# Kernel tuning notes

Hardware: AMD Instinct MI355X
Metric: run time of the kernel (lower is better)

Reference implementation:

```python
import jax, jax.numpy as jnp
import numpy as np

N = 50000

def gcn_conv(x, W, b, src, dst, n):
    # x: [N, Fin], W: [Fin, Fout]; PyG GCNConv: transform then sym-normalized aggregate (self-loops included in src/dst)
    h = x @ W  # [N, Fout]
    deg = jax.ops.segment_sum(jnp.ones_like(dst, dtype=h.dtype), dst, num_segments=n)
    inv_sqrt = jnp.where(deg > 0, jax.lax.rsqrt(deg), 0.0)
    norm = inv_sqrt[src] * inv_sqrt[dst]  # [E+N]
    msg = h[src] * norm[:, None]
    out = jax.ops.segment_sum(msg, dst, num_segments=n)
    return out + b


def setup_inputs() -> dict:
    key = jax.random.key(0)
    ks = jax.random.split(key, 8)
    d_in, d_h, n_exp, E = 64, 64, 16, 800000
    x = jax.random.normal(ks[0], (N, d_in), dtype=jnp.float32)
    edge_index = jax.random.randint(ks[1], (2, E), 0, N, dtype=jnp.int64)
    s = 1.0 / np.sqrt(d_in)
    W1 = jax.random.uniform(ks[2], (d_in, d_h), minval=-s, maxval=s, dtype=jnp.float32)
    b1 = jnp.zeros((d_h,), jnp.float32)
    W2 = jax.random.uniform(ks[3], (d_h, d_h), minval=-s, maxval=s, dtype=jnp.float32)
    b2 = jnp.zeros((d_h,), jnp.float32)
    Wc = jax.random.uniform(ks[4], (d_h, n_exp), minval=-s, maxval=s, dtype=jnp.float32)
    bc = jnp.zeros((n_exp,), jnp.float32)
    return {"x": x, "edge_index": edge_index, "W1": W1, "b1": b1, "W2": W2, "b2": b2, "Wc": Wc, "bc": bc}


def reference(x, edge_index, W1, b1, W2, b2, Wc, bc):
    # add self-loops once (PyG GCNConv default add_self_loops=True)
    loops = jnp.arange(N, dtype=edge_index.dtype)
    src = jnp.concatenate([edge_index[0], loops])
    dst = jnp.concatenate([edge_index[1], loops])
    h = jax.nn.relu(gcn_conv(x, W1, b1, src, dst, N))
    # dropout is identity in eval mode
    h = jax.nn.relu(gcn_conv(h, W2, b2, src, dst, N))
    return h @ Wc + bc
```

## Files before the change

### kernel.cpp

```cpp
#include <hip/hip_runtime.h>
#include <hip/hip_fp16.h>


#define FDIM 64
#define NCLS 16
#define TILE 2048

__global__ __launch_bounds__(256) void k_histB(const int* __restrict__ dst, int E,
                                               int* __restrict__ H) {
    __shared__ int h[256];
    int t = threadIdx.x, blk = blockIdx.x;
    h[t] = 0;
    __syncthreads();
    int i0 = blk * TILE;
#pragma unroll
    for (int k = 0; k < TILE / 256; ++k) {
        int i = i0 + k * 256 + t;
        if (i < E) atomicAdd(&h[dst[i] >> 8], 1);
    }
    __syncthreads();
    H[blk * 256 + t] = h[t];
}

__global__ __launch_bounds__(512) void k_scanH(int* __restrict__ H, int nblk, int* __restrict__ btot) {
    __shared__ int s[512];
    int t = threadIdx.x, b = blockIdx.x;
    int v = (t < nblk) ? H[t * 256 + b] : 0;
    s[t] = v;
    __syncthreads();
    for (int off = 1; off < 512; off <<= 1) {
        int add = (t >= off) ? s[t - off] : 0;
        __syncthreads();
        s[t] += add;
        __syncthreads();
    }
    if (t < nblk) H[t * 256 + b] = s[t] - v;
    if (t == 511) btot[b] = s[511];
}

__global__ __launch_bounds__(256) void k_scatA(const int* __restrict__ src, const int* __restrict__ dst,
                                               int E, const int* __restrict__ H,
                                               const int* __restrict__ btot, int nb,
                                               unsigned* __restrict__ tmp) {
    __shared__ int s[256];
    __shared__ int Hb[256];
    __shared__ int c2[256];
    int t = threadIdx.x, blk = blockIdx.x;
    int v = (t < nb) ? btot[t] : 0;
    s[t] = v;
    __syncthreads();
    for (int off = 1; off < 256; off <<= 1) {
        int add = (t >= off) ? s[t - off] : 0;
        __syncthreads();
        s[t] += add;
        __syncthreads();
    }
    Hb[t] = (s[t] - v) + H[blk * 256 + t];
    c2[t] = 0;
    __syncthreads();
    int i0 = blk * TILE;
#pragma unroll
    for (int k = 0; k < TILE / 256; ++k) {
        int i = i0 + k * 256 + t;
        if (i < E) {
            int sv = src[i], d = dst[i];
            int b = d >> 8;
            unsigned rec = ((unsigned)(d & 255) << 16) | (unsigned)sv;
            int pos = Hb[b] + atomicAdd(&c2[b], 1);
            tmp[pos] = rec;
        }
    }
}

#define COLCAP 8192
__global__ __launch_bounds__(256) void k_binB(const unsigned* __restrict__ tmp,
                                              const int* __restrict__ btot, int nb,
                                              int n, int E, int* __restrict__ row_ptr,
                                              float* __restrict__ inv,
                                              unsigned short* __restrict__ col) {
    __shared__ int dcnt[256], s[256], cur[256];
    __shared__ unsigned short colbuf[COLCAP];
    int t = threadIdx.x, b = blockIdx.x;
    int v = (t < nb) ? btot[t] : 0;
    s[t] = v;
    __syncthreads();
    for (int off = 1; off < 256; off <<= 1) {
        int add = (t >= off) ? s[t - off] : 0;
        __syncthreads();
        s[t] += add;
        __syncthreads();
    }
    __shared__ int baseS;
    if (t == b) baseS = s[t] - v;
    dcnt[t] = 0;
    __syncthreads();
    int base = baseS;
    int cntE = btot[b];
    int node0 = b << 8;
    int nn = min(256, n - node0);
    for (int i = t; i < cntE; i += 256) atomicAdd(&dcnt[tmp[base + i] >> 16], 1);
    __syncthreads();
    int deg = dcnt[t];
    s[t] = deg;
    __syncthreads();
    for (int off = 1; off < 256; off <<= 1) {
        int add = (t >= off) ? s[t - off] : 0;
        __syncthreads();
        s[t] += add;
        __syncthreads();
    }
    int excl = s[t] - deg;
    if (t < nn) {
        row_ptr[node0 + t] = base + excl;
        inv[node0 + t] = rsqrtf((float)(deg + 1));
    }
    if (b == 0 && t == 0) row_ptr[n] = E;
    cur[t] = excl;
    __syncthreads();
    for (int i = t; i < cntE; i += 256) {
        unsigned r = tmp[base + i];
        int pos = atomicAdd(&cur[r >> 16], 1);
        unsigned short vv = (unsigned short)(r & 0xFFFFu);
        if (pos < COLCAP) colbuf[pos] = vv;
        else col[base + pos] = vv;
    }
    __syncthreads();
    int lim = min(cntE, COLCAP);
    for (int i = t; i < lim; i += 256) col[base + i] = colbuf[i];
}

__global__ __launch_bounds__(256) void k_gemm64(const float* __restrict__ X, const float* __restrict__ W,
                                                const float* __restrict__ inv, __half* __restrict__ Yh, int n) {
    __shared__ float Ws[FDIM * FDIM];
    int t = threadIdx.x;
    for (int i = t; i < FDIM * FDIM; i += 256) Ws[i] = W[i];
    __syncthreads();
    int idx = blockIdx.x * 256 + t;
    int row = idx >> 2;
    int cg = (idx & 3) * 16;
    if (row >= n) return;
    const float4* xr = (const float4*)(X + row * FDIM);
    float4 xv[16];
#pragma unroll
    for (int i = 0; i < 16; ++i) xv[i] = xr[i];
    float acc[16];
#pragma unroll
    for (int c = 0; c < 16; ++c) acc[c] = 0.f;
#pragma unroll
    for (int i = 0; i < 16; ++i) {
        float xs[4] = {xv[i].x, xv[i].y, xv[i].z, xv[i].w};
#pragma unroll
        for (int j = 0; j < 4; ++j) {
            float xk = xs[j];
            const float* wr = &Ws[(i * 4 + j) * FDIM + cg];
#pragma unroll
            for (int c = 0; c < 16; ++c) acc[c] += xk * wr[c];
        }
    }
    float iv = inv[row];
    unsigned u[8];
#pragma unroll
    for (int i = 0; i < 8; ++i) {
        __half2 hp = __floats2half2_rn(acc[2 * i] * iv, acc[2 * i + 1] * iv);
        u[i] = *(unsigned*)&hp;
    }
    uint4* yo = (uint4*)(Yh + (size_t)row * FDIM + cg);
    yo[0] = make_uint4(u[0], u[1], u[2], u[3]);
    yo[1] = make_uint4(u[4], u[5], u[6], u[7]);
}

__global__ __launch_bounds__(256) void k_aggF1(const __half* __restrict__ Ph, const float* __restrict__ inv,
                                               const int* __restrict__ row_ptr,
                                               const unsigned short* __restrict__ col,
                                               const float* __restrict__ bias,
                                               const float* __restrict__ W2,
                                               __half* __restrict__ P2, int n) {
    __shared__ float W2s[FDIM * FDIM];
    __shared__ float rbuf[16][FDIM + 1];
    int t = threadIdx.x;
    for (int i = t; i < FDIM * FDIM; i += 256) W2s[i] = W2[i];
    int lane = t & 63;
    int sub = lane >> 4;
    int fl = lane & 15;
    int wid = t >> 6;
    int nl = wid * 4 + sub;
    int node = blockIdx.x * 16 + nl;
    bool alive = node < n;
    int nodeC = alive ? node : (n - 1);
    float iv = inv[nodeC];
    const uint2* Pq = (const uint2*)Ph;
    uint2 selfq = Pq[(size_t)nodeC * 16 + fl];
    float2 sf0 = __half22float2(*(__half2*)&selfq.x);
    float2 sf1 = __half22float2(*(__half2*)&selfq.y);
    float4 acc = make_float4(sf0.x, sf0.y, sf1.x, sf1.y);
    int s = row_ptr[nodeC];
    int e = alive ? row_ptr[nodeC + 1] : s;
    int dmax = e - s;
    dmax = max(dmax, __shfl_xor(dmax, 16, 64));
    dmax = max(dmax, __shfl_xor(dmax, 32, 64));
    for (int j = 0; j < dmax; j += 8) {
        int c[8];
        float wk[8];
        uint2 q[8];
#pragma unroll
        for (int k = 0; k < 8; ++k) {
            int jj = s + j + k;
            bool ok = jj < e;
            c[k] = col[ok ? jj : s];
            wk[k] = ok ? 1.f : 0.f;
        }
#pragma unroll
        for (int k = 0; k < 8; ++k) q[k] = Pq[(size_t)c[k] * 16 + fl];
#pragma unroll
        for (int k = 0; k < 8; ++k) {
            float2 f0 = __half22float2(*(__half2*)&q[k].x);
            float2 f1 = __half22float2(*(__half2*)&q[k].y);
            acc.x = fmaf(wk[k], f0.x, acc.x);
            acc.y = fmaf(wk[k], f0.y, acc.y);
            acc.z = fmaf(wk[k], f1.x, acc.z);
            acc.w = fmaf(wk[k], f1.y, acc.w);
        }
    }
    float4 bb = ((const float4*)bias)[fl];
    rbuf[nl][fl * 4 + 0] = fmaxf(fmaf(iv, acc.x, bb.x), 0.f);
    rbuf[nl][fl * 4 + 1] = fmaxf(fmaf(iv, acc.y, bb.y), 0.f);
    rbuf[nl][fl * 4 + 2] = fmaxf(fmaf(iv, acc.z, bb.z), 0.f);
    rbuf[nl][fl * 4 + 3] = fmaxf(fmaf(iv, acc.w, bb.w), 0.f);
    __syncthreads();
    int nl2 = t >> 4;
    int cg = t & 15;
    int node2 = blockIdx.x * 16 + nl2;
    const float* rr = rbuf[nl2];
    float a0 = 0.f, a1 = 0.f, a2 = 0.f, a3 = 0.f;
#pragma unroll
    for (int i = 0; i < FDIM; ++i) {
        float xk = rr[i];
        const float* wv = &W2s[i * FDIM + cg * 4];
        a0 = fmaf(xk, wv[0], a0);
        a1 = fmaf(xk, wv[1], a1);
        a2 = fmaf(xk, wv[2], a2);
        a3 = fmaf(xk, wv[3], a3);
    }
    if (node2 < n) {
        float iv2 = inv[node2];
        __half2 h0 = __floats2half2_rn(a0 * iv2, a1 * iv2);
        __half2 h1 = __floats2half2_rn(a2 * iv2, a3 * iv2);
        uint2 val = make_uint2(*(unsigned*)&h0, *(unsigned*)&h1);
        ((uint2*)P2)[(size_t)node2 * 16 + cg] = val;
    }
}

__global__ __launch_bounds__(256) void k_aggF2(const __half* __restrict__ Ph, const float* __restrict__ inv,
                                               const int* __restrict__ row_ptr,
                                               const unsigned short* __restrict__ col,
                                               const float* __restrict__ bias,
                                               const float* __restrict__ Wc, const float* __restrict__ bc,
                                               float* __restrict__ out, int n) {
    __shared__ float WcT[NCLS * FDIM];
    int t = threadIdx.x;
    for (int i = t; i < FDIM * NCLS; i += 256) {
        int c = i & 15, f = i >> 4;
        WcT[c * FDIM + f] = Wc[i];
    }
    __syncthreads();
    int lane = t & 63;
    int sub = lane >> 4;
    int fl = lane & 15;
    int wid = t >> 6;
    int node = blockIdx.x * 16 + wid * 4 + sub;
    bool alive = node < n;
    int nodeC = alive ? node : (n - 1);
    float iv = inv[nodeC];
    const uint2* Pq = (const uint2*)Ph;
    uint2 selfq = Pq[(size_t)nodeC * 16 + fl];
    float2 sf0 = __half22float2(*(__half2*)&selfq.x);
    float2 sf1 = __half22float2(*(__half2*)&selfq.y);
    float4 acc = make_float4(sf0.x, sf0.y, sf1.x, sf1.y);
    int s = row_ptr[nodeC];
    int e = alive ? row_ptr[nodeC + 1] : s;
    int dmax = e - s;
    dmax = max(dmax, __shfl_xor(dmax, 16, 64));
    dmax = max(dmax, __shfl_xor(dmax, 32, 64));
    for (int j = 0; j < dmax; j += 8) {
        int c[8];
        float wk[8];
        uint2 q[8];
#pragma unroll
        for (int k = 0; k < 8; ++k) {
            int jj = s + j + k;
            bool ok = jj < e;
            c[k] = col[ok ? jj : s];
            wk[k] = ok ? 1.f : 0.f;
        }
#pragma unroll
        for (int k = 0; k < 8; ++k) q[k] = Pq[(size_t)c[k] * 16 + fl];
#pragma unroll
        for (int k = 0; k < 8; ++k) {
            float2 f0 = __half22float2(*(__half2*)&q[k].x);
            float2 f1 = __half22float2(*(__half2*)&q[k].y);
            acc.x = fmaf(wk[k], f0.x, acc.x);
            acc.y = fmaf(wk[k], f0.y, acc.y);
            acc.z = fmaf(wk[k], f1.x, acc.z);
            acc.w = fmaf(wk[k], f1.y, acc.w);
        }
    }
    float4 bb = ((const float4*)bias)[fl];
    float4 r;
    r.x = fmaxf(fmaf(iv, acc.x, bb.x), 0.f);
    r.y = fmaxf(fmaf(iv, acc.y, bb.y), 0.f);
    r.z = fmaxf(fmaf(iv, acc.z, bb.z), 0.f);
    r.w = fmaxf(fmaf(iv, acc.w, bb.w), 0.f);
    float part[NCLS];
#pragma unroll
    for (int c = 0; c < NCLS; ++c) {
        float4 wv = ((const float4*)(WcT + c * FDIM))[fl];
        part[c] = fmaf(r.x, wv.x, fmaf(r.y, wv.y, fmaf(r.z, wv.z, r.w * wv.w)));
    }
#pragma unroll
    for (int m = 1; m < 16; m <<= 1) {
#pragma unroll
        for (int c = 0; c < NCLS; ++c) part[c] += __shfl_xor(part[c], m, 64);
    }
    if (alive && fl < 4) {
        float4 bb2 = ((const float4*)bc)[fl];
        float4 o = make_float4(part[fl * 4 + 0] + bb2.x, part[fl * 4 + 1] + bb2.y,
                               part[fl * 4 + 2] + bb2.z, part[fl * 4 + 3] + bb2.w);
        ((float4*)out)[(size_t)node * 4 + fl] = o;
    }
}

static inline size_t align256(size_t x) { return (x + 255) & ~(size_t)255; }

extern "C" void kernel_launch(void* const* d_in, const int* in_sizes, int n_in,
                              void* d_out, int out_size, void* d_ws, size_t ws_size,
                              hipStream_t stream) {
    const float* x  = (const float*)d_in[0];
    const int*   ei = (const int*)d_in[1];
    const float* W1 = (const float*)d_in[2];
    const float* b1 = (const float*)d_in[3];
    const float* W2 = (const float*)d_in[4];
    const float* b2 = (const float*)d_in[5];
    const float* Wc = (const float*)d_in[6];
    const float* bc = (const float*)d_in[7];
    float* out = (float*)d_out;

    const int n = in_sizes[0] / FDIM;
    const int E = in_sizes[1] / 2;
    const int* src = ei;
    const int* dst = ei + E;

    const int nb = (n + 255) >> 8;
    const int nblk = (E + TILE - 1) / TILE;

    char* w = (char*)d_ws;
    size_t off = 0;
    int* H = (int*)(w + off);        off = align256(off + (size_t)nblk * 256 * 4);
    int* btot = (int*)(w + off);     off = align256(off + 256 * 4);
    int* row_ptr = (int*)(w + off);  off = align256(off + (size_t)(n + 1) * 4);
    float* inv = (float*)(w + off);  off = align256(off + (size_t)n * 4);
    unsigned* tmp = (unsigned*)(w + off);             off = align256(off + (size_t)E * 4);
    unsigned short* col = (unsigned short*)(w + off); off = align256(off + (size_t)(E + 8) * 2);
    __half* P1 = (__half*)(w + off); off = align256(off + (size_t)n * FDIM * 2);
    __half* P2 = (__half*)(w + off); off = align256(off + (size_t)n * FDIM * 2);
    (void)ws_size;

    const int nbG = (n * 4 + 255) / 256;
    const int nbA = (n + 15) / 16;

    k_histB<<<nblk, 256, 0, stream>>>(dst, E, H);
    k_scanH<<<nb, 512, 0, stream>>>(H, nblk, btot);
    k_scatA<<<nblk, 256, 0, stream>>>(src, dst, E, H, btot, nb, tmp);
    k_binB<<<nb, 256, 0, stream>>>(tmp, btot, nb, n, E, row_ptr, inv, col);

    k_gemm64<<<nbG, 256, 0, stream>>>(x, W1, inv, P1, n);
    k_aggF1<<<nbA, 256, 0, stream>>>(P1, inv, row_ptr, col, b1, W2, P2, n);
    k_aggF2<<<nbA, 256, 0, stream>>>(P2, inv, row_ptr, col, b2, Wc, bc, out, n);
}
```

Before: 162.8 us.

## Merge first-layer GEMM into histogram kernel, apply source normalization in aggregation

The first GEMM no longer scales rows by inv-sqrt degree, so it no longer depends on the CSR build. It is folded into the histogram launch as extra blocks, letting GEMM work overlap the edge histogram and removing one launch. In exchange, the first aggregation now gathers inv[c] for every neighbor edge, adding a random 4-byte load per edge. Both aggregation loops also drop the wavefront-wide max-degree shuffle and loop per 16-lane group on its own degree, so lanes within a wave may diverge.

```diff
diff --git a/kernel.cpp b/kernel.cpp
--- a/kernel.cpp
+++ b/kernel.cpp
@@ -6,20 +6,60 @@
 #define NCLS 16
 #define TILE 2048
 
-__global__ __launch_bounds__(256) void k_histB(const int* __restrict__ dst, int E,
-                                               int* __restrict__ H) {
+__global__ __launch_bounds__(256) void k_histgemm(const int* __restrict__ dst, int E,
+                                                  int* __restrict__ H, int nblk,
+                                                  const float* __restrict__ X,
+                                                  const float* __restrict__ W,
+                                                  __half* __restrict__ Yh, int n) {
+    __shared__ float Ws[FDIM * FDIM];
     __shared__ int h[256];
     int t = threadIdx.x, blk = blockIdx.x;
-    h[t] = 0;
-    __syncthreads();
-    int i0 = blk * TILE;
-#pragma unroll
-    for (int k = 0; k < TILE / 256; ++k) {
-        int i = i0 + k * 256 + t;
-        if (i < E) atomicAdd(&h[dst[i] >> 8], 1);
-    }
-    __syncthreads();
-    H[blk * 256 + t] = h[t];
+    if (blk < nblk) {
+        h[t] = 0;
+        __syncthreads();
+        int i0 = blk * TILE;
+#pragma unroll
+        for (int k = 0; k < TILE / 256; ++k) {
+            int i = i0 + k * 256 + t;
+            if (i < E) atomicAdd(&h[dst[i] >> 8], 1);
+        }
+        __syncthreads();
+        H[blk * 256 + t] = h[t];
+    } else {
+        for (int i = t; i < FDIM * FDIM; i += 256) Ws[i] = W[i];
+        __syncthreads();
+        int idx = (blk - nblk) * 256 + t;
+        int row = idx >> 2;
+        int cg = (idx & 3) * 16;
+        if (row >= n) return;
+        const float4* xr = (const float4*)(X + (size_t)row * FDIM);
+        float4 xv[16];
+#pragma unroll
+        for (int i = 0; i < 16; ++i) xv[i] = xr[i];
+        float acc[16];
+#pragma unroll
+        for (int c = 0; c < 16; ++c) acc[c] = 0.f;
+#pragma unroll
+        for (int i = 0; i < 16; ++i) {
+            float xs[4] = {xv[i].x, xv[i].y, xv[i].z, xv[i].w};
+#pragma unroll
+            for (int j = 0; j < 4; ++j) {
+                float xk = xs[j];
+                const float* wr = &Ws[(i * 4 + j) * FDIM + cg];
+#pragma unroll
+                for (int c = 0; c < 16; ++c) acc[c] += xk * wr[c];
+            }
+        }
+        unsigned u[8];
+#pragma unroll
+        for (int i = 0; i < 8; ++i) {
+            __half2 hp = __floats2half2_rn(acc[2 * i], acc[2 * i + 1]);
+            u[i] = *(unsigned*)&hp;
+        }
+        uint4* yo = (uint4*)(Yh + (size_t)row * FDIM + cg);
+        yo[0] = make_uint4(u[0], u[1], u[2], u[3]);
+        yo[1] = make_uint4(u[4], u[5], u[6], u[7]);
+    }
 }
 
 __global__ __launch_bounds__(512) void k_scanH(int* __restrict__ H, int nblk, int* __restrict__ btot) {
@@ -127,46 +167,6 @@
     __syncthreads();
     int lim = min(cntE, COLCAP);
     for (int i = t; i < lim; i += 256) col[base + i] = colbuf[i];
-}
-
-__global__ __launch_bounds__(256) void k_gemm64(const float* __restrict__ X, const float* __restrict__ W,
-                                                const float* __restrict__ inv, __half* __restrict__ Yh, int n) {
-    __shared__ float Ws[FDIM * FDIM];
-    int t = threadIdx.x;
-    for (int i = t; i < FDIM * FDIM; i += 256) Ws[i] = W[i];
-    __syncthreads();
-    int idx = blockIdx.x * 256 + t;
-    int row = idx >> 2;
-    int cg = (idx & 3) * 16;
-    if (row >= n) return;
-    const float4* xr = (const float4*)(X + row * FDIM);
-    float4 xv[16];
-#pragma unroll
-    for (int i = 0; i < 16; ++i) xv[i] = xr[i];
-    float acc[16];
-#pragma unroll
-    for (int c = 0; c < 16; ++c) acc[c] = 0.f;
-#pragma unroll
-    for (int i = 0; i < 16; ++i) {
-        float xs[4] = {xv[i].x, xv[i].y, xv[i].z, xv[i].w};
-#pragma unroll
-        for (int j = 0; j < 4; ++j) {
-            float xk = xs[j];
-            const float* wr = &Ws[(i * 4 + j) * FDIM + cg];
-#pragma unroll
-            for (int c = 0; c < 16; ++c) acc[c] += xk * wr[c];
-        }
-    }
-    float iv = inv[row];
-    unsigned u[8];
-#pragma unroll
-    for (int i = 0; i < 8; ++i) {
-        __half2 hp = __floats2half2_rn(acc[2 * i] * iv, acc[2 * i + 1] * iv);
-        u[i] = *(unsigned*)&hp;
-    }
-    uint4* yo = (uint4*)(Yh + (size_t)row * FDIM + cg);
-    yo[0] = make_uint4(u[0], u[1], u[2], u[3]);
-    yo[1] = make_uint4(u[4], u[5], u[6], u[7]);
 }
 
 __global__ __launch_bounds__(256) void k_aggF1(const __half* __restrict__ Ph, const float* __restrict__ inv,
@@ -192,23 +192,21 @@
     uint2 selfq = Pq[(size_t)nodeC * 16 + fl];
     float2 sf0 = __half22float2(*(__half2*)&selfq.x);
     float2 sf1 = __half22float2(*(__half2*)&selfq.y);
-    float4 acc = make_float4(sf0.x, sf0.y, sf1.x, sf1.y);
+    float4 acc = make_float4(iv * sf0.x, iv * sf0.y, iv * sf1.x, iv * sf1.y);
     int s = row_ptr[nodeC];
     int e = alive ? row_ptr[nodeC + 1] : s;
-    int dmax = e - s;
-    dmax = max(dmax, __shfl_xor(dmax, 16, 64));
-    dmax = max(dmax, __shfl_xor(dmax, 32, 64));
-    for (int j = 0; j < dmax; j += 8) {
+    for (int j = s; j < e; j += 8) {
         int c[8];
         float wk[8];
         uint2 q[8];
 #pragma unroll
         for (int k = 0; k < 8; ++k) {
-            int jj = s + j + k;
+            int jj = j + k;
             bool ok = jj < e;
             c[k] = col[ok ? jj : s];
-            wk[k] = ok ? 1.f : 0.f;
-        }
+        }
+#pragma unroll
+        for (int k = 0; k < 8; ++k) wk[k] = ((j + k) < e) ? inv[c[k]] : 0.f;
 #pragma unroll
         for (int k = 0; k < 8; ++k) q[k] = Pq[(size_t)c[k] * 16 + fl];
 #pragma unroll
@@ -278,16 +276,13 @@
     float4 acc = make_float4(sf0.x, sf0.y, sf1.x, sf1.y);
     int s = row_ptr[nodeC];
     int e = alive ? row_ptr[nodeC + 1] : s;
-    int dmax = e - s;
-    dmax = max(dmax, __shfl_xor(dmax, 16, 64));
-    dmax = max(dmax, __shfl_xor(dmax, 32, 64));
-    for (int j = 0; j < dmax; j += 8) {
+    for (int j = s; j < e; j += 8) {
         int c[8];
         float wk[8];
         uint2 q[8];
 #pragma unroll
         for (int k = 0; k < 8; ++k) {
-            int jj = s + j + k;
+            int jj = j + k;
             bool ok = jj < e;
             c[k] = col[ok ? jj : s];
             wk[k] = ok ? 1.f : 0.f;
@@ -367,12 +362,11 @@
     const int nbG = (n * 4 + 255) / 256;
     const int nbA = (n + 15) / 16;
 
-    k_histB<<<nblk, 256, 0, stream>>>(dst, E, H);
+    k_histgemm<<<nblk + nbG, 256, 0, stream>>>(dst, E, H, nblk, x, W1, P1, n);
     k_scanH<<<nb, 512, 0, stream>>>(H, nblk, btot);
     k_scatA<<<nblk, 256, 0, stream>>>(src, dst, E, H, btot, nb, tmp);
     k_binB<<<nb, 256, 0, stream>>>(tmp, btot, nb, n, E, row_ptr, inv, col);
 
-    k_gemm64<<<nbG, 256, 0, stream>>>(x, W1, inv, P1, n);
     k_aggF1<<<nbA, 256, 0, stream>>>(P1, inv, row_ptr, col, b1, W2, P2, n);
     k_aggF2<<<nbA, 256, 0, stream>>>(P2, inv, row_ptr, col, b2, Wc, bc, out, n);
 }
```

New measurement: 161.5 us. About the same (-0.8%).
